# Optimization experiments

Measured on AMD Instinct MI355X. Metric: run time of the kernel, lower is better.

Reference implementation:

```python
import jax, jax.numpy as jnp
import numpy as np

B, L, D_MODEL = 8, 2048, 512
N_QUBITS, Q_LAYERS = 10, 4
DIM = 2 ** N_QUBITS
EPS = 1e-5  # torch LayerNorm default


def _apply_1q_tok(state, U, q):
    # per-token 2x2 gate U: (N,2,2), wire 0 = most significant (PennyLane order)
    N = state.shape[0]
    s = state.reshape(N, 2 ** q, 2, -1)
    return jnp.einsum('nij,najb->naib', U, s).reshape(N, -1)


def _apply_1q(state, U, q):
    # shared 2x2 gate U: (2,2)
    N = state.shape[0]
    s = state.reshape(N, 2 ** q, 2, -1)
    return jnp.einsum('ij,najb->naib', U, s).reshape(N, -1)


def _cnot(state, c, t):
    N = state.shape[0]
    lo, hi = min(c, t), max(c, t)
    s = state.reshape(N, 2 ** lo, 2, 2 ** (hi - lo - 1), 2, -1)
    if c < t:
        # control is the first 2-axis; flip target axis where control==1
        s = s.at[:, :, 1].set(jnp.flip(s[:, :, 1], axis=3))
    else:
        # target is the first 2-axis, control the second
        s = s.at[:, :, :, :, 1].set(jnp.flip(s[:, :, :, :, 1], axis=2))
    return s.reshape(N, -1)


def _simulate(feats, weights):
    # feats: (N, n_qubits) angles; weights: (q_layers, n_qubits, 2)
    N = feats.shape[0]
    half = 0.5 * feats
    cxa = jnp.cos(half).astype(jnp.complex64)
    sxa = jnp.sin(half).astype(jnp.complex64)
    phz = jnp.exp(1j * half.astype(jnp.complex64))  # e^{+i theta/2}
    state = jnp.zeros((N, DIM), jnp.complex64).at[:, 0].set(1.0 + 0j)
    for l in range(Q_LAYERS):
        # AngleEmbedding rotation='X' : RX(feat_q) on wire q
        for q in range(N_QUBITS):
            c, s = cxa[:, q], sxa[:, q]
            U = jnp.stack([jnp.stack([c, -1j * s], -1),
                           jnp.stack([-1j * s, c], -1)], -2)  # (N,2,2)
            state = _apply_1q_tok(state, U, q)
        # AngleEmbedding rotation='Z' : RZ(feat_q) on wire q (diagonal)
        for q in range(N_QUBITS):
            p = phz[:, q]
            diag = jnp.stack([jnp.conj(p), p], -1)  # (N,2)
            s = state.reshape(N, 2 ** q, 2, -1)
            state = (s * diag[:, None, :, None]).reshape(N, -1)
        # trainable RY, RZ per wire (shared across tokens)
        for q in range(N_QUBITS):
            ty = 0.5 * weights[l, q, 0]
            cy, sy = jnp.cos(ty), jnp.sin(ty)
            Uy = jnp.stack([jnp.stack([cy, -sy]), jnp.stack([sy, cy])]).astype(jnp.complex64)
            state = _apply_1q(state, Uy, q)
            pz = jnp.exp(1j * (0.5 * weights[l, q, 1]).astype(jnp.complex64))
            diag = jnp.stack([jnp.conj(pz), pz])  # (2,)
            s = state.reshape(N, 2 ** q, 2, -1)
            state = (s * diag[None, None, :, None]).reshape(N, -1)
        # entangling CNOT ring
        for q in range(N_QUBITS):
            state = _cnot(state, q, (q + 1) % N_QUBITS)
    probs = jnp.real(state) ** 2 + jnp.imag(state) ** 2  # (N, 2**n)
    zs = []
    for q in range(N_QUBITS):
        p = probs.reshape(N, 2 ** q, 2, -1).sum(axis=(1, 3))  # (N,2)
        zs.append(p[:, 0] - p[:, 1])  # <Z_q>
    return jnp.stack(zs, -1)  # (N, n_qubits)


def setup_inputs() -> dict:
    key = jax.random.key(0)
    ks = jax.random.split(key, 4)
    x = jax.random.normal(ks[0], (B, L, D_MODEL), jnp.float32)
    in_W = jax.random.normal(ks[1], (N_QUBITS, D_MODEL), jnp.float32) / np.float32(np.sqrt(D_MODEL))
    in_b = jnp.zeros((N_QUBITS,), jnp.float32)
    gamma = jnp.ones((N_QUBITS,), jnp.float32)
    beta = jnp.zeros((N_QUBITS,), jnp.float32)
    weights = 0.05 * jax.random.normal(ks[2], (Q_LAYERS, N_QUBITS, 2), jnp.float32)
    out_W = jax.random.normal(ks[3], (D_MODEL, N_QUBITS), jnp.float32) / np.float32(np.sqrt(N_QUBITS))
    out_b = jnp.zeros((D_MODEL,), jnp.float32)
    return {"x": x, "in_W": in_W, "in_b": in_b, "gamma": gamma, "beta": beta,
            "weights": weights, "out_W": out_W, "out_b": out_b}


def reference(x, in_W, in_b, gamma, beta, weights, out_W, out_b):
    Bs, Ls, _ = x.shape
    h = jnp.tanh(jnp.einsum('bld,qd->blq', x, in_W) + in_b)
    mu = h.mean(-1, keepdims=True)
    var = ((h - mu) ** 2).mean(-1, keepdims=True)
    h = (h - mu) / jnp.sqrt(var + EPS) * gamma + beta
    q_out = _simulate(h.reshape(Bs * Ls, N_QUBITS), weights)
    q_out = q_out.reshape(Bs, Ls, N_QUBITS).astype(x.dtype)
    return x + jnp.einsum('blq,dq->bld', q_out, out_W) + out_b
```

## Files before the change

### kernel.cpp

```cpp
#include <hip/hip_runtime.h>

#define NQ 10
#define DQ 512
#define QL 4
#define NTOK (8 * 2048)
#define QOFF (NQ * DQ)
#define QHOFF (QOFF + 480)

typedef float v2f __attribute__((ext_vector_type(2)));
typedef float v4f __attribute__((ext_vector_type(4)));
typedef _Float16 h2 __attribute__((ext_vector_type(2)));

__device__ __forceinline__ int bperm(int addr, int v) {
    return __builtin_amdgcn_ds_bpermute(addr, v);
}
__device__ __forceinline__ float bpermf(int addr, float v) {
    return __builtin_bit_cast(float, bperm(addr, __builtin_bit_cast(int, v)));
}
__device__ __forceinline__ h2 bpermh(int addr, h2 v) {
    return __builtin_bit_cast(h2, bperm(addr, __builtin_bit_cast(int, v)));
}
template <int CTRL>
__device__ __forceinline__ int dppi(int i) {
    return __builtin_amdgcn_update_dpp(i, i, CTRL, 0xF, 0xF, false);
}
template <int M>
__device__ __forceinline__ float dppxf(float v) {
    int i = __builtin_bit_cast(int, v);
    if constexpr (M == 1)      i = dppi<0xB1>(i);
    else if constexpr (M == 2) i = dppi<0x4E>(i);
    else                       i = dppi<0x128>(i);
    return __builtin_bit_cast(float, i);
}
template <int M>
__device__ __forceinline__ h2 dppxh(h2 v) {
    int i = __builtin_bit_cast(int, v);
    if constexpr (M == 1)      i = dppi<0xB1>(i);
    else if constexpr (M == 2) i = dppi<0x4E>(i);
    else                       i = dppi<0x128>(i);
    return __builtin_bit_cast(h2, i);
}

template <int N>
__device__ __forceinline__ void reduceNf(float* z, int a32, int a16, int a4) {
#pragma unroll
    for (int q = 0; q < N; ++q) {
        z[q] += bpermf(a32, z[q]);
        z[q] += bpermf(a16, z[q]);
        z[q] += dppxf<8>(z[q]);
        z[q] += bpermf(a4, z[q]);
        z[q] += dppxf<2>(z[q]);
        z[q] += dppxf<1>(z[q]);
    }
}

__device__ __forceinline__ h2 pk2(float a, float b) {
    return __builtin_bit_cast(h2, __builtin_amdgcn_cvt_pkrtz(a, b));
}
__device__ __forceinline__ h2 h2swap(h2 v) {
    return __builtin_shufflevector(v, v, 1, 0);
}
__device__ __forceinline__ h2 splat_lo(h2 v) {
    return __builtin_shufflevector(v, v, 0, 0);
}
__device__ __forceinline__ h2 splat_hi(h2 v) {
    return __builtin_shufflevector(v, v, 1, 1);
}

__device__ __forceinline__ v4f coef(const v4f* Q, float A, float C) {
    return Q[0] + A * Q[1] + C * Q[2];
}
__device__ __forceinline__ void coefh2(const h2* Qg6, const h2 AC[2][NQ], int q,
                                       h2* arai, h2* brbi) {
    const h2 q0 = Qg6[0], q1 = Qg6[1], q2 = Qg6[2];
    const h2 q3 = Qg6[3], q4 = Qg6[4], q5 = Qg6[5];
#pragma unroll
    for (int tt = 0; tt < 2; ++tt) {
        h2 A2 = splat_lo(AC[tt][q]), C2 = splat_hi(AC[tt][q]);
        arai[tt] = q0 + A2 * q2 + C2 * q4;
        brbi[tt] = q1 + A2 * q3 + C2 * q5;
    }
}

__device__ __forceinline__ void gate_lane_hp2(h2 (&sr)[2][8], h2 (&si)[2][8],
                                              const h2* arai, const h2* brbi,
                                              bool bit, int addr) {
    h2 ar[2], br[2], bi[2], Ai[2], Br[2];
#pragma unroll
    for (int tt = 0; tt < 2; ++tt) {
        ar[tt] = splat_lo(arai[tt]);
        h2 ai = splat_hi(arai[tt]);
        br[tt] = splat_lo(brbi[tt]);
        bi[tt] = splat_hi(brbi[tt]);
        Ai[tt] = bit ? -ai : ai;
        Br[tt] = bit ? br[tt] : -br[tt];
    }
#pragma unroll
    for (int j = 0; j < 8; ++j)
#pragma unroll
        for (int tt = 0; tt < 2; ++tt) {
            h2 wr = bpermh(addr, sr[tt][j]), wi = bpermh(addr, si[tt][j]);
            h2 nr = ar[tt] * sr[tt][j] - Ai[tt] * si[tt][j] + Br[tt] * wr - bi[tt] * wi;
            h2 ni = ar[tt] * si[tt][j] + Ai[tt] * sr[tt][j] + Br[tt] * wi + bi[tt] * wr;
            sr[tt][j] = nr; si[tt][j] = ni;
        }
}
template <int M>
__device__ __forceinline__ void gate_lane_hd2(h2 (&sr)[2][8], h2 (&si)[2][8],
                                              const h2* arai, const h2* brbi,
                                              bool bit) {
    h2 ar[2], br[2], bi[2], Ai[2], Br[2];
#pragma unroll
    for (int tt = 0; tt < 2; ++tt) {
        ar[tt] = splat_lo(arai[tt]);
        h2 ai = splat_hi(arai[tt]);
        br[tt] = splat_lo(brbi[tt]);
        bi[tt] = splat_hi(brbi[tt]);
        Ai[tt] = bit ? -ai : ai;
        Br[tt] = bit ? br[tt] : -br[tt];
    }
#pragma unroll
    for (int j = 0; j < 8; ++j)
#pragma unroll
        for (int tt = 0; tt < 2; ++tt) {
            h2 wr = dppxh<M>(sr[tt][j]), wi = dppxh<M>(si[tt][j]);
            h2 nr = ar[tt] * sr[tt][j] - Ai[tt] * si[tt][j] + Br[tt] * wr - bi[tt] * wi;
            h2 ni = ar[tt] * si[tt][j] + Ai[tt] * sr[tt][j] + Br[tt] * wi + bi[tt] * wr;
            sr[tt][j] = nr; si[tt][j] = ni;
        }
}
template <int BJ>
__device__ __forceinline__ void gate_reg_h2(h2 (&sr)[2][8], h2 (&si)[2][8],
                                            const h2* arai, const h2* brbi) {
#pragma unroll
    for (int tt = 0; tt < 2; ++tt) {
        const h2 ar = splat_lo(arai[tt]), ai = splat_hi(arai[tt]);
        const h2 br = splat_lo(brbi[tt]), bi = splat_hi(brbi[tt]);
#pragma unroll
        for (int j = 0; j < 8; ++j) if (!(j & BJ)) {
            const int j1 = j | BJ;
            h2 x0r = sr[tt][j], x0i = si[tt][j];
            h2 x1r = sr[tt][j1], x1i = si[tt][j1];
            sr[tt][j]  = ar * x0r - ai * x0i - br * x1r - bi * x1i;
            si[tt][j]  = ar * x0i + ai * x0r - br * x1i + bi * x1r;
            sr[tt][j1] = br * x0r - bi * x0i + ar * x1r + ai * x1i;
            si[tt][j1] = br * x0i + bi * x0r + ar * x1i - ai * x1r;
        }
    }
}
__device__ __forceinline__ void gate_elem_h2(h2 (&sr)[2][8], h2 (&si)[2][8],
                                             const h2* arai, const h2* brbi) {
#pragma unroll
    for (int tt = 0; tt < 2; ++tt) {
        const h2 ar = splat_lo(arai[tt]), bi = splat_hi(brbi[tt]);
        const h2 aiV = __builtin_bit_cast(h2,
            __builtin_bit_cast(int, splat_hi(arai[tt])) ^ (int)0x80000000);
        const h2 brV = __builtin_bit_cast(h2,
            __builtin_bit_cast(int, splat_lo(brbi[tt])) ^ 0x00008000);
#pragma unroll
        for (int j = 0; j < 8; ++j) {
            h2 swr = h2swap(sr[tt][j]), swi = h2swap(si[tt][j]);
            h2 nr = ar * sr[tt][j] - aiV * si[tt][j] + brV * swr - bi * swi;
            h2 ni = ar * si[tt][j] + aiV * sr[tt][j] + brV * swi + bi * swr;
            sr[tt][j] = nr; si[tt][j] = ni;
        }
    }
}

__device__ __forceinline__ void perm678_h(h2* a) {
    h2 o2 = a[2], o4 = a[4], o7 = a[7];
    a[1] = h2swap(a[1]);
    a[2] = a[3]; a[3] = h2swap(o2);
    a[4] = a[6]; a[6] = a[5]; a[5] = h2swap(o7); a[7] = h2swap(o4);
}

__device__ __forceinline__ void cnot_ring2(h2 (&sr)[2][8], h2 (&si)[2][8],
                                           int lane, int apm, int a32) {
#pragma unroll
    for (int j = 0; j < 8; ++j)
#pragma unroll
        for (int tt = 0; tt < 2; ++tt) {
            sr[tt][j] = bpermh(apm, sr[tt][j]);
            si[tt][j] = bpermh(apm, si[tt][j]);
        }
    {
        const bool ctrl = (lane & 1);
#pragma unroll
        for (int tt = 0; tt < 2; ++tt)
#pragma unroll
            for (int j = 0; j < 4; ++j) {
                h2 t0 = sr[tt][j], t1 = sr[tt][j + 4];
                sr[tt][j] = ctrl ? t1 : t0; sr[tt][j + 4] = ctrl ? t0 : t1;
                t0 = si[tt][j]; t1 = si[tt][j + 4];
                si[tt][j] = ctrl ? t1 : t0; si[tt][j + 4] = ctrl ? t0 : t1;
            }
    }
#pragma unroll
    for (int tt = 0; tt < 2; ++tt) {
        perm678_h(sr[tt]);
        perm678_h(si[tt]);
    }
#pragma unroll
    for (int j = 0; j < 8; ++j)
#pragma unroll
        for (int tt = 0; tt < 2; ++tt) {
            h2 w = bpermh(a32, sr[tt][j]); sr[tt][j] = (h2){sr[tt][j].x, w.y};
            w = bpermh(a32, si[tt][j]);    si[tt][j] = (h2){si[tt][j].x, w.y};
        }
}

__device__ __forceinline__ void build_product(h2* sr, h2* si, const v4f* Q0,
                                              const float* Aq, const float* Cq,
                                              int lane) {
    v4f f0 = coef(Q0 + 0, Aq[0], Cq[0]);
    bool b0 = (lane & 32);
    float Lr = b0 ? f0.z : f0.x, Li = b0 ? f0.w : f0.y;
#pragma unroll
    for (int q = 1; q < 6; ++q) {
        v4f f = coef(Q0 + 3 * q, Aq[q], Cq[q]);
        bool b = lane & (1 << (5 - q));
        float fr = b ? f.z : f.x, fi = b ? f.w : f.y;
        float nr = Lr * fr - Li * fi, ni = Lr * fi + Li * fr;
        Lr = nr; Li = ni;
    }
    float Pr[8], Pi[8];
    {
        v4f f6 = coef(Q0 + 18, Aq[6], Cq[6]);
        Pr[0] = Lr * f6.x - Li * f6.y; Pi[0] = Lr * f6.y + Li * f6.x;
        Pr[4] = Lr * f6.z - Li * f6.w; Pi[4] = Lr * f6.w + Li * f6.z;
    }
    {
        v4f f7 = coef(Q0 + 21, Aq[7], Cq[7]);
#pragma unroll
        for (int jj = 0; jj < 8; jj += 4) {
            float tr1 = Pr[jj] * f7.z - Pi[jj] * f7.w;
            float ti1 = Pr[jj] * f7.w + Pi[jj] * f7.z;
            float tr0 = Pr[jj] * f7.x - Pi[jj] * f7.y;
            float ti0 = Pr[jj] * f7.y + Pi[jj] * f7.x;
            Pr[jj] = tr0; Pi[jj] = ti0; Pr[jj + 2] = tr1; Pi[jj + 2] = ti1;
        }
    }
    {
        v4f f8 = coef(Q0 + 24, Aq[8], Cq[8]);
#pragma unroll
        for (int jj = 0; jj < 8; jj += 2) {
            float tr1 = Pr[jj] * f8.z - Pi[jj] * f8.w;
            float ti1 = Pr[jj] * f8.w + Pi[jj] * f8.z;
            float tr0 = Pr[jj] * f8.x - Pi[jj] * f8.y;
            float ti0 = Pr[jj] * f8.y + Pi[jj] * f8.x;
            Pr[jj] = tr0; Pi[jj] = ti0; Pr[jj + 1] = tr1; Pi[jj + 1] = ti1;
        }
    }
    {
        v4f f9 = coef(Q0 + 27, Aq[9], Cq[9]);
#pragma unroll
        for (int j = 0; j < 8; ++j) {
            float e0r = Pr[j] * f9.x - Pi[j] * f9.y;
            float e0i = Pr[j] * f9.y + Pi[j] * f9.x;
            float e1r = Pr[j] * f9.z - Pi[j] * f9.w;
            float e1i = Pr[j] * f9.w + Pi[j] * f9.z;
            sr[j] = pk2(e0r, e1r);
            si[j] = pk2(e0i, e1i);
        }
    }
}

__global__ __launch_bounds__(512) void prep_kernel(
    const float* __restrict__ weights, const float* __restrict__ out_W,
    float* __restrict__ ws)
{
    const int t = threadIdx.x;
#pragma unroll
    for (int q = 0; q < NQ; ++q)
        ws[q * DQ + t] = out_W[t * NQ + q];
    if (t < QL * NQ) {
        float w0 = weights[t * 2], w1 = weights[t * 2 + 1];
        float cy = __cosf(0.5f * w0), sy = __sinf(0.5f * w0);
        float cz = __cosf(0.5f * w1), sz = __sinf(0.5f * w1);
        float d = cy - sy, e = cy + sy;
        v4f q0 = (v4f){-cz * sy,  sz * sy,  cz * cy,  sz * cy};
        v4f q1 = (v4f){ cz * e,  -sz * e,  -cz * d,  -sz * d};
        v4f q2 = (v4f){-sz * d,  -cz * d,   sz * e,  -cz * e};
        v4f* Q = (v4f*)(ws + QOFF);
        Q[t * 3 + 0] = q0; Q[t * 3 + 1] = q1; Q[t * 3 + 2] = q2;
        h2* Qh = (h2*)(ws + QHOFF);
        Qh[t * 6 + 0] = pk2(q0.x, q0.y); Qh[t * 6 + 1] = pk2(q0.z, q0.w);
        Qh[t * 6 + 2] = pk2(q1.x, q1.y); Qh[t * 6 + 3] = pk2(q1.z, q1.w);
        Qh[t * 6 + 4] = pk2(q2.x, q2.y); Qh[t * 6 + 5] = pk2(q2.z, q2.w);
    }
}

__global__ __launch_bounds__(256) void quantum_kernel(
    const float* __restrict__ x, const float* __restrict__ in_W,
    const float* __restrict__ in_b, const float* __restrict__ gamma,
    const float* __restrict__ beta, const float* __restrict__ ws,
    const float* __restrict__ out_b, float* __restrict__ out)
{
    const int t = threadIdx.x;
    const int lane = t & 63;
    const int tok0 = (blockIdx.x * 4 + (t >> 6)) * 2;
    const v4f* Qg = (const v4f*)(ws + QOFF);
    const h2*  Qh = (const h2*)(ws + QHOFF);

    const int a32 = (lane ^ 32) << 2;
    const int a16 = (lane ^ 16) << 2;
    const int a4  = (lane ^ 4)  << 2;
    int srcl = lane;
#pragma unroll
    for (int q = 4; q >= 0; --q) {
        const int bc = 5 - q, bt = bc - 1;
        srcl ^= ((srcl >> bc) & 1) << bt;
    }
    const int apm = srcl << 2;

    const v4f* xr0 = (const v4f*)(x + (size_t)tok0 * DQ);
    const v4f* xr1 = (const v4f*)(x + (size_t)(tok0 + 1) * DQ);
    const v4f* inW4 = (const v4f*)in_W;
    const v4f xk00 = xr0[lane], xk01 = xr0[lane + 64];
    const v4f xk10 = xr1[lane], xk11 = xr1[lane + 64];
    float h[2][NQ];
#pragma unroll
    for (int q = 0; q < NQ; ++q) {
        v4f w0 = inW4[q * (DQ / 4) + lane];
        v4f w1 = inW4[q * (DQ / 4) + lane + 64];
        v4f a0 = xk00 * w0 + xk01 * w1;
        v4f a1 = xk10 * w0 + xk11 * w1;
        h[0][q] = (a0.x + a0.y) + (a0.z + a0.w);
        h[1][q] = (a1.x + a1.y) + (a1.z + a1.w);
    }
    reduceNf<2 * NQ>(&h[0][0], a32, a16, a4);

    h2 AC[2][NQ];
    h2 sr[2][8], si[2][8];
#pragma unroll
    for (int tt = 0; tt < 2; ++tt) {
        float mu = 0.f;
#pragma unroll
        for (int q = 0; q < NQ; ++q) {
            float e = __expf(2.f * (h[tt][q] + in_b[q]));
            h[tt][q] = (e - 1.f) * __builtin_amdgcn_rcpf(e + 1.f);
            mu += h[tt][q];
        }
        mu *= 0.1f;
        float var = 0.f;
#pragma unroll
        for (int q = 0; q < NQ; ++q) { float d0 = h[tt][q] - mu; var += d0 * d0; }
        var *= 0.1f;
        const float rstd = rsqrtf(var + 1e-5f);

        float Aq[NQ], Cq[NQ];
#pragma unroll
        for (int q = 0; q < NQ; ++q) {
            float f = (h[tt][q] - mu) * rstd * gamma[q] + beta[q];
            float hf = 0.5f * f;
            float c = __cosf(hf), s = __sinf(hf);
            Aq[q] = c * c;
            Cq[q] = c * s;
            AC[tt][q] = pk2(Aq[q], Cq[q]);
        }
        build_product(sr[tt], si[tt], Qg, Aq, Cq, lane);
    }
    cnot_ring2(sr, si, lane, apm, a32);

#pragma unroll 1
    for (int l = 1; l < QL; ++l) {
        const h2* Ql = Qh + l * NQ * 6;
        h2 arai[2], brbi[2];
        coefh2(Ql + 0 * 6, AC, 0, arai, brbi); gate_lane_hp2(sr, si, arai, brbi, lane & 32, a32);
        coefh2(Ql + 2 * 6, AC, 2, arai, brbi); gate_lane_hd2<8>(sr, si, arai, brbi, lane & 8);
        coefh2(Ql + 1 * 6, AC, 1, arai, brbi); gate_lane_hp2(sr, si, arai, brbi, lane & 16, a16);
        coefh2(Ql + 4 * 6, AC, 4, arai, brbi); gate_lane_hd2<2>(sr, si, arai, brbi, lane & 2);
        coefh2(Ql + 3 * 6, AC, 3, arai, brbi); gate_lane_hp2(sr, si, arai, brbi, lane & 4, a4);
        coefh2(Ql + 5 * 6, AC, 5, arai, brbi); gate_lane_hd2<1>(sr, si, arai, brbi, lane & 1);
        coefh2(Ql + 6 * 6, AC, 6, arai, brbi); gate_reg_h2<4>(sr, si, arai, brbi);
        coefh2(Ql + 7 * 6, AC, 7, arai, brbi); gate_reg_h2<2>(sr, si, arai, brbi);
        coefh2(Ql + 8 * 6, AC, 8, arai, brbi); gate_reg_h2<1>(sr, si, arai, brbi);
        coefh2(Ql + 9 * 6, AC, 9, arai, brbi); gate_elem_h2(sr, si, arai, brbi);
        if (l < QL - 1) cnot_ring2(sr, si, lane, apm, a32);
    }

    const bool P1 = __popc(lane & 0x30) & 1;
    const bool P2 = __popc(lane & 0x38) & 1;
    const bool P3 = __popc(lane & 0x3C) & 1;
    const bool P4 = __popc(lane & 0x3E) & 1;
    const bool P5 = __popc(lane & 0x3F) & 1;
    const bool PX = __popc(lane & 0x1F) & 1;
    h2 zp[10];
#pragma unroll
    for (int tt = 0; tt < 2; ++tt) {
        h2 aP = (h2){0, 0}, a6 = (h2){0, 0}, a7 = (h2){0, 0}, aT = (h2){0, 0};
#pragma unroll
        for (int j = 0; j < 8; ++j) {
            h2 p = sr[tt][j] * sr[tt][j] + si[tt][j] * si[tt][j];
            aP += p;
            if (j & 4) a6 -= p; else a6 += p;
            if (((j >> 2) ^ (j >> 1)) & 1) a7 -= p; else a7 += p;
            if (((j >> 2) ^ (j >> 1) ^ j) & 1) aT -= p; else aT += p;
        }
        const float A0 = (float)aP.x + (float)aP.y;
        const float B6 = (float)a6.x + (float)a6.y;
        const float B7 = (float)a7.x + (float)a7.y;
        const float B8 = (float)aT.x + (float)aT.y;
        const float B9 = (float)aT.x - (float)aT.y;
        float z[NQ];
        z[0] = PX ? -B9 : B9;
        z[1] = P1 ? -A0 : A0;
        z[2] = P2 ? -A0 : A0;
        z[3] = P3 ? -A0 : A0;
        z[4] = P4 ? -A0 : A0;
        z[5] = P5 ? -A0 : A0;
        z[6] = P5 ? -B6 : B6;
        z[7] = P5 ? -B7 : B7;
        z[8] = P5 ? -B8 : B8;
        z[9] = P5 ? -B9 : B9;
#pragma unroll
        for (int i = 0; i < 5; ++i) zp[tt * 5 + i] = pk2(z[2 * i], z[2 * i + 1]);
    }

#pragma unroll
    for (int i = 0; i < 10; ++i) {
        zp[i] += bpermh(a32, zp[i]);
        zp[i] += bpermh(a16, zp[i]);
        zp[i] += dppxh<8>(zp[i]);
        zp[i] += bpermh(a4, zp[i]);
        zp[i] += dppxh<2>(zp[i]);
        zp[i] += dppxh<1>(zp[i]);
    }
    float zf[2][NQ];
#pragma unroll
    for (int tt = 0; tt < 2; ++tt)
#pragma unroll
        for (int i = 0; i < 5; ++i) {
            zf[tt][2 * i]     = (float)zp[tt * 5 + i].x;
            zf[tt][2 * i + 1] = (float)zp[tt * 5 + i].y;
        }

    v4f* or0 = (v4f*)(out + (size_t)tok0 * DQ);
    v4f* or1 = (v4f*)(out + (size_t)(tok0 + 1) * DQ);
    const v4f* ob4 = (const v4f*)out_b;
    const v4f* oWt4 = (const v4f*)ws;
#pragma unroll
    for (int k = 0; k < 2; ++k) {
        const int d4 = lane + 64 * k;
        const v4f b = ob4[d4];
        v4f acc0 = xr0[d4] + b;
        v4f acc1 = xr1[d4] + b;
#pragma unroll
        for (int q = 0; q < NQ; ++q) {
            v4f w = oWt4[q * (DQ / 4) + d4];
            acc0 = zf[0][q] * w + acc0;
            acc1 = zf[1][q] * w + acc1;
        }
        or0[d4] = acc0;
        or1[d4] = acc1;
    }
}

extern "C" void kernel_launch(void* const* d_in, const int* in_sizes, int n_in,
                              void* d_out, int out_size, void* d_ws, size_t ws_size,
                              hipStream_t stream) {
    const float* x       = (const float*)d_in[0];
    const float* in_W    = (const float*)d_in[1];
    const float* in_b    = (const float*)d_in[2];
    const float* gamma   = (const float*)d_in[3];
    const float* beta    = (const float*)d_in[4];
    const float* weights = (const float*)d_in[5];
    const float* out_W   = (const float*)d_in[6];
    const float* out_b   = (const float*)d_in[7];
    float* out = (float*)d_out;
    float* ws = (float*)d_ws;

    hipLaunchKernelGGL(prep_kernel, dim3(1), dim3(512), 0, stream,
                       weights, out_W, ws);
    hipLaunchKernelGGL(quantum_kernel, dim3(NTOK / 8), dim3(256), 0, stream,
                       x, in_W, in_b, gamma, beta, ws, out_b, out);
}
```

Measured before the change: 193.3 us.

## Fuse prep kernel into quantum kernel, staging out_W and gate coefficients in LDS

Removes the separate one-block prep launch. Each block now computes the trainable-gate coefficients itself and transposes out_W into shared memory, then synchronises before the main simulation. This saves a kernel launch and the serial dependency between the two kernels. In exchange, every one of the 2048 blocks redoes the transpose and the trig work, and takes about 20KB of LDS, which may lower occupancy.

```diff
diff --git a/kernel.cpp b/kernel.cpp
--- a/kernel.cpp
+++ b/kernel.cpp
@@ -4,8 +4,6 @@
 #define DQ 512
 #define QL 4
 #define NTOK (8 * 2048)
-#define QOFF (NQ * DQ)
-#define QHOFF (QOFF + 480)
 
 typedef float v2f __attribute__((ext_vector_type(2)));
 typedef float v4f __attribute__((ext_vector_type(4)));
@@ -265,14 +263,21 @@
     }
 }
 
-__global__ __launch_bounds__(512) void prep_kernel(
-    const float* __restrict__ weights, const float* __restrict__ out_W,
-    float* __restrict__ ws)
+__global__ __launch_bounds__(256) void quantum_kernel(
+    const float* __restrict__ x, const float* __restrict__ in_W,
+    const float* __restrict__ in_b, const float* __restrict__ gamma,
+    const float* __restrict__ beta, const float* __restrict__ weights,
+    const float* __restrict__ out_W, const float* __restrict__ out_b,
+    float* __restrict__ out)
 {
     const int t = threadIdx.x;
-#pragma unroll
-    for (int q = 0; q < NQ; ++q)
-        ws[q * DQ + t] = out_W[t * NQ + q];
+    const int lane = t & 63;
+    const int tok0 = (blockIdx.x * 4 + (t >> 6)) * 2;
+
+    __shared__ float outW_lds[NQ * DQ];
+    __shared__ v4f   Qg_lds[NQ * 3];
+    __shared__ h2    Qh_lds[QL * NQ * 6];
+
     if (t < QL * NQ) {
         float w0 = weights[t * 2], w1 = weights[t * 2 + 1];
         float cy = __cosf(0.5f * w0), sy = __sinf(0.5f * w0);
@@ -281,26 +286,23 @@
         v4f q0 = (v4f){-cz * sy,  sz * sy,  cz * cy,  sz * cy};
         v4f q1 = (v4f){ cz * e,  -sz * e,  -cz * d,  -sz * d};
         v4f q2 = (v4f){-sz * d,  -cz * d,   sz * e,  -cz * e};
-        v4f* Q = (v4f*)(ws + QOFF);
-        Q[t * 3 + 0] = q0; Q[t * 3 + 1] = q1; Q[t * 3 + 2] = q2;
-        h2* Qh = (h2*)(ws + QHOFF);
-        Qh[t * 6 + 0] = pk2(q0.x, q0.y); Qh[t * 6 + 1] = pk2(q0.z, q0.w);
-        Qh[t * 6 + 2] = pk2(q1.x, q1.y); Qh[t * 6 + 3] = pk2(q1.z, q1.w);
-        Qh[t * 6 + 4] = pk2(q2.x, q2.y); Qh[t * 6 + 5] = pk2(q2.z, q2.w);
-    }
-}
-
-__global__ __launch_bounds__(256) void quantum_kernel(
-    const float* __restrict__ x, const float* __restrict__ in_W,
-    const float* __restrict__ in_b, const float* __restrict__ gamma,
-    const float* __restrict__ beta, const float* __restrict__ ws,
-    const float* __restrict__ out_b, float* __restrict__ out)
-{
-    const int t = threadIdx.x;
-    const int lane = t & 63;
-    const int tok0 = (blockIdx.x * 4 + (t >> 6)) * 2;
-    const v4f* Qg = (const v4f*)(ws + QOFF);
-    const h2*  Qh = (const h2*)(ws + QHOFF);
+        Qh_lds[t * 6 + 0] = pk2(q0.x, q0.y); Qh_lds[t * 6 + 1] = pk2(q0.z, q0.w);
+        Qh_lds[t * 6 + 2] = pk2(q1.x, q1.y); Qh_lds[t * 6 + 3] = pk2(q1.z, q1.w);
+        Qh_lds[t * 6 + 4] = pk2(q2.x, q2.y); Qh_lds[t * 6 + 5] = pk2(q2.z, q2.w);
+        if (t < NQ) {
+            Qg_lds[t * 3 + 0] = q0; Qg_lds[t * 3 + 1] = q1; Qg_lds[t * 3 + 2] = q2;
+        }
+    }
+#pragma unroll
+    for (int d = t; d < DQ; d += 256) {
+#pragma unroll
+        for (int q = 0; q < NQ; ++q)
+            outW_lds[q * DQ + d] = out_W[d * NQ + q];
+    }
+    __syncthreads();
+
+    const v4f* Qg = (const v4f*)Qg_lds;
+    const h2*  Qh = (const h2*)Qh_lds;
 
     const int a32 = (lane ^ 32) << 2;
     const int a16 = (lane ^ 16) << 2;
@@ -438,7 +440,7 @@
     v4f* or0 = (v4f*)(out + (size_t)tok0 * DQ);
     v4f* or1 = (v4f*)(out + (size_t)(tok0 + 1) * DQ);
     const v4f* ob4 = (const v4f*)out_b;
-    const v4f* oWt4 = (const v4f*)ws;
+    const v4f* oWt4 = (const v4f*)outW_lds;
 #pragma unroll
     for (int k = 0; k < 2; ++k) {
         const int d4 = lane + 64 * k;
@@ -468,10 +470,7 @@
     const float* out_W   = (const float*)d_in[6];
     const float* out_b   = (const float*)d_in[7];
     float* out = (float*)d_out;
-    float* ws = (float*)d_ws;
-
-    hipLaunchKernelGGL(prep_kernel, dim3(1), dim3(512), 0, stream,
-                       weights, out_W, ws);
+
     hipLaunchKernelGGL(quantum_kernel, dim3(NTOK / 8), dim3(256), 0, stream,
-                       x, in_W, in_b, gamma, beta, ws, out_b, out);
-}
+                       x, in_W, in_b, gamma, beta, weights, out_W, out_b, out);
+}
```

Result: slower. 207.6 us (+7.4%).
